# Kernel optimization log

Measured on AMD Instinct MI355X. Metric: run time of the kernel, lower is better.

Reference implementation:

```python
import jax, jax.numpy as jnp
import numpy as np

# loss hyperparameters (module defaults)
ATTENTION_COEFF = 1.0
GAMMA = 0.5
BETA = 8.0
DICE_COEFF = 2500.0
REV_DICE_COEFF = 2500.0
IOU_COEFF = 0.0
EPS = 1e-14
SMOOTH = 1e-6
LOG_CLAMP = -100.0  # torch F.binary_cross_entropy clamps log terms at -100


def setup_inputs() -> dict:
    key = jax.random.key(0)
    k1, k2 = jax.random.split(key)
    B, C, H, W = 16, 4, 512, 512
    cls_score = jax.random.uniform(k1, (B, C, H, W), dtype=jnp.float32)
    label = jax.random.randint(k2, (B, C, H, W), 0, 2, dtype=jnp.int32)
    return {"cls_score": cls_score, "label": label}


def _attention_bce(pred, t):
    # per-batch alpha = num_neg / total over all 4 channels (vectorized over batch)
    num_pos = jnp.sum(t, axis=(1, 2, 3))                      # (B,)
    total = jnp.float32(t.shape[1] * t.shape[2] * t.shape[3])
    alpha = ((total - num_pos) / total)[:, None, None, None]  # (B,1,1,1)
    p_clip = jnp.clip(pred, EPS, 1.0 - EPS)
    # beta ** ((1-p)**gamma) and beta ** (p**gamma)
    w = (t * alpha * BETA ** ((1.0 - p_clip) ** GAMMA)
         + (1.0 - t) * (1.0 - alpha) * BETA ** (p_clip ** GAMMA))
    w = jax.lax.stop_gradient(w)
    # BCE on raw pred, with torch-style log clamping
    log_p = jnp.maximum(jnp.log(pred), LOG_CLAMP)
    log_1mp = jnp.maximum(jnp.log(1.0 - pred), LOG_CLAMP)
    bce = -(t * log_p + (1.0 - t) * log_1mp)
    return jnp.sum(w * bce)


def _dice(pred, t):
    inter = jnp.sum(pred * t, axis=(2, 3))                    # (B,4)
    denom = jnp.sum(pred * pred, axis=(2, 3)) + jnp.sum(t * t, axis=(2, 3))
    return jnp.sum(1.0 - (2.0 * inter + SMOOTH) / (denom + SMOOTH))


def _iou(pred, t):
    inter = jnp.sum(pred * t, axis=(2, 3))
    union = jnp.sum(pred + t, axis=(2, 3)) - inter
    return jnp.sum(1.0 - (inter + SMOOTH) / (union + SMOOTH))


def reference(cls_score, label):
    t = label.astype(jnp.float32)  # (B,4,H,W)
    loss = ATTENTION_COEFF * _attention_bce(cls_score, t)
    loss = loss + DICE_COEFF * _dice(cls_score, t)
    loss = loss + REV_DICE_COEFF * _dice(1.0 - cls_score, 1.0 - t)
    loss = loss + IOU_COEFF * _iou(cls_score, t)
    return loss
```

## Files before the change

### kernel.cpp

```cpp
#include <hip/hip_runtime.h>


typedef float f32x4 __attribute__((ext_vector_type(4)));
typedef int   i32x4 __attribute__((ext_vector_type(4)));

#define B_DIM 16
#define C_DIM 4
#define HW 262144
#define NPLANES 64
#define NTHREADS 128
#define NWAVES (NTHREADS / 64)
#define CHUNK 2048
#define K_CHUNKS (HW / CHUNK)
#define NBLOCKS (NPLANES * K_CHUNKS)
#define NSUMS 6
#define WELEMS (CHUNK / NWAVES)
#define WOPS (WELEMS / 256)

__global__ __launch_bounds__(NTHREADS) void loss_main(
    const float* __restrict__ pred, const int* __restrict__ label,
    float* __restrict__ ws) {
  __shared__ float sp[NWAVES][WELEMS];
  __shared__ int   st[NWAVES][WELEMS];
  __shared__ float red[NWAVES][NSUMS];

  const int block = blockIdx.x;
  const int tid = threadIdx.x;
  const int w = tid >> 6, l = tid & 63;
  const long wbase = (long)block * CHUNK + (long)w * WELEMS;
  const float* gp = pred + wbase;
  const int*   gt = label + wbase;

#pragma unroll
  for (int r = 0; r < WOPS; ++r) {
    __builtin_amdgcn_global_load_lds(
        (const __attribute__((address_space(1))) void*)(gp + r * 256 + l * 4),
        (__attribute__((address_space(3))) void*)(&sp[w][r * 256]), 16, 0, 0);
    __builtin_amdgcn_global_load_lds(
        (const __attribute__((address_space(1))) void*)(gt + r * 256 + l * 4),
        (__attribute__((address_space(3))) void*)(&st[w][r * 256]), 16, 0, 0);
  }
  __syncthreads();

  float s_pt = 0.f, s_pp = 0.f, s_p = 0.f;
  float nsum_t = 0.f;
  float nsum_1 = 0.f;
  int   s_ti = 0;

#pragma unroll
  for (int r = 0; r < WOPS; ++r) {
    f32x4 P = *(const f32x4*)&sp[w][r * 256 + l * 4];
    i32x4 T = *(const i32x4*)&st[w][r * 256 + l * 4];
#pragma unroll
    for (int j = 0; j < 4; ++j) {
      float pv = P[j];
      float tf = (float)T[j];
      float u   = __builtin_fmaf(tf, -2.0f, 1.0f);
      float arg = __builtin_fmaf(pv, u, tf);
      float x   = 1.0f - arg;
      float r_  = __builtin_amdgcn_sqrtf(x);
      float Bw  = __builtin_amdgcn_exp2f(3.0f * r_);
      float lg  = __builtin_amdgcn_logf(arg);
      float L   = fmaxf(0.69314718056f * lg, -100.0f);
      float c   = Bw * (-L);
      nsum_t += c;
      nsum_1  = __builtin_fmaf(tf, c, nsum_1);
      s_pt    = __builtin_fmaf(tf, pv, s_pt);
      s_pp    = __builtin_fmaf(pv, pv, s_pp);
      s_p    += pv;
      s_ti   += T[j];
    }
  }

  float s_t = (float)s_ti;

  float vals[NSUMS] = {s_pt, s_pp, s_t, s_p, nsum_1, nsum_t};
#pragma unroll
  for (int q = 0; q < NSUMS; ++q) {
    float v = vals[q];
#pragma unroll
    for (int off = 32; off; off >>= 1) v += __shfl_down(v, off);
    vals[q] = v;
  }
  if (l == 0) {
#pragma unroll
    for (int q = 0; q < NSUMS; ++q) red[w][q] = vals[q];
  }
  __syncthreads();
  if (tid < NSUMS) {
    float v = 0.f;
#pragma unroll
    for (int ww = 0; ww < NWAVES; ++ww) v += red[ww][tid];
    ws[block * NSUMS + tid] = v;
  }
}

__global__ __launch_bounds__(1024) void loss_finalize(
    const float* __restrict__ ws, float* __restrict__ out) {
  __shared__ float ps[NPLANES][NSUMS];
  const int tid = threadIdx.x;
  const int p = tid >> 4;
  const int s = tid & 15;

  float acc[NSUMS] = {0.f, 0.f, 0.f, 0.f, 0.f, 0.f};
  const f32x4* base =
      (const f32x4*)(ws + (long)p * (K_CHUNKS * NSUMS) + s * 48);
#pragma unroll
  for (int i = 0; i < 12; ++i) {
    f32x4 v = base[i];
#pragma unroll
    for (int j = 0; j < 4; ++j) acc[(i * 4 + j) % 6] += v[j];
  }
#pragma unroll
  for (int q = 0; q < NSUMS; ++q) {
    float v = acc[q];
    v += __shfl_xor(v, 1);
    v += __shfl_xor(v, 2);
    v += __shfl_xor(v, 4);
    v += __shfl_xor(v, 8);
    acc[q] = v;
  }
  if (s == 0) {
#pragma unroll
    for (int q = 0; q < NSUMS; ++q) ps[p][q] = acc[q];
  }
  __syncthreads();

  if (tid < 64) {
    const int pl = tid;
    const float s_pt = ps[pl][0], s_pp = ps[pl][1], s_t = ps[pl][2],
                s_p = ps[pl][3];
    const float sum1 = ps[pl][4];
    const float sum2 = ps[pl][5] - ps[pl][4];
    const float N = (float)HW;
    const float SM = 1e-6f;

    float dice = 1.0f - (2.0f * s_pt + SM) / (s_pp + s_t + SM);
    float inter2 = N - s_p - s_t + s_pt;
    float denom2 = 2.0f * N - 2.0f * s_p + s_pp - s_t;
    float rdice = 1.0f - (2.0f * inter2 + SM) / (denom2 + SM);

    float np4 = s_t + __shfl_xor(s_t, 1);
    np4 += __shfl_xor(np4, 2);
    const float total = (float)(C_DIM * HW);
    float alpha = (total - np4) / total;

    float val = alpha * sum1 + (1.0f - alpha) * sum2
              + 2500.0f * (dice + rdice);

#pragma unroll
    for (int off = 32; off; off >>= 1) val += __shfl_down(val, off);
    if (pl == 0) out[0] = val;
  }
}

extern "C" void kernel_launch(void* const* d_in, const int* in_sizes, int n_in,
                              void* d_out, int out_size, void* d_ws, size_t ws_size,
                              hipStream_t stream) {
  const float* pred = (const float*)d_in[0];
  const int* label = (const int*)d_in[1];
  float* out = (float*)d_out;
  float* ws = (float*)d_ws;

  loss_main<<<NBLOCKS, NTHREADS, 0, stream>>>(pred, label, ws);
  loss_finalize<<<1, 1024, 0, stream>>>(ws, out);
}
```

Before: 31.18 us.

## Double-buffer LDS tiles so each block streams four chunks

Each block now processes four 2048-element tiles instead of one. Asynchronous global-to-LDS loads feed two LDS buffers, so the next tile's loads are in flight while the current tile is computed. This cuts the block count by four and shrinks the per-plane partial-sum array the finalize kernel reduces. In exchange, per-block LDS doubles to about 32KB, which limits how many blocks fit on a CU. The barrier at the end of each iteration may also serialize the loads and the compute.

```diff
diff --git a/kernel.cpp b/kernel.cpp
--- a/kernel.cpp
+++ b/kernel.cpp
@@ -10,67 +10,88 @@
 #define NPLANES 64
 #define NTHREADS 128
 #define NWAVES (NTHREADS / 64)
-#define CHUNK 2048
-#define K_CHUNKS (HW / CHUNK)
-#define NBLOCKS (NPLANES * K_CHUNKS)
+#define TILE 2048
+#define TILES 4
+#define NBLOCKS 2048
+#define BPP 32
 #define NSUMS 6
-#define WELEMS (CHUNK / NWAVES)
+#define WELEMS (TILE / NWAVES)
 #define WOPS (WELEMS / 256)
 
 __global__ __launch_bounds__(NTHREADS) void loss_main(
     const float* __restrict__ pred, const int* __restrict__ label,
     float* __restrict__ ws) {
-  __shared__ float sp[NWAVES][WELEMS];
-  __shared__ int   st[NWAVES][WELEMS];
+  __shared__ float sp[2][TILE];
+  __shared__ int   st[2][TILE];
   __shared__ float red[NWAVES][NSUMS];
 
   const int block = blockIdx.x;
   const int tid = threadIdx.x;
   const int w = tid >> 6, l = tid & 63;
-  const long wbase = (long)block * CHUNK + (long)w * WELEMS;
-  const float* gp = pred + wbase;
-  const int*   gt = label + wbase;
+  const long base0 = (long)block * (TILE * TILES);
+  const float* gp = pred + base0 + w * WELEMS;
+  const int*   gt = label + base0 + w * WELEMS;
 
-#pragma unroll
-  for (int r = 0; r < WOPS; ++r) {
-    __builtin_amdgcn_global_load_lds(
-        (const __attribute__((address_space(1))) void*)(gp + r * 256 + l * 4),
-        (__attribute__((address_space(3))) void*)(&sp[w][r * 256]), 16, 0, 0);
-    __builtin_amdgcn_global_load_lds(
-        (const __attribute__((address_space(1))) void*)(gt + r * 256 + l * 4),
-        (__attribute__((address_space(3))) void*)(&st[w][r * 256]), 16, 0, 0);
+#define STAGE(c, t)                                                          \
+  _Pragma("unroll")                                                          \
+  for (int r = 0; r < WOPS; ++r) {                                           \
+    __builtin_amdgcn_global_load_lds(                                        \
+        (const __attribute__((address_space(1))) void*)(gp + (t) * TILE +    \
+                                                        r * 256 + l * 4),    \
+        (__attribute__((address_space(3))) void*)(&sp[c][w * WELEMS +        \
+                                                         r * 256]),          \
+        16, 0, 0);                                                           \
+    __builtin_amdgcn_global_load_lds(                                        \
+        (const __attribute__((address_space(1))) void*)(gt + (t) * TILE +    \
+                                                        r * 256 + l * 4),    \
+        (__attribute__((address_space(3))) void*)(&st[c][w * WELEMS +        \
+                                                         r * 256]),          \
+        16, 0, 0);                                                           \
   }
-  __syncthreads();
 
   float s_pt = 0.f, s_pp = 0.f, s_p = 0.f;
   float nsum_t = 0.f;
   float nsum_1 = 0.f;
   int   s_ti = 0;
 
+#define COMPUTE(c)                                                           \
+  _Pragma("unroll")                                                          \
+  for (int r = 0; r < WOPS; ++r) {                                           \
+    f32x4 P = *(const f32x4*)&sp[c][w * WELEMS + r * 256 + l * 4];           \
+    i32x4 T = *(const i32x4*)&st[c][w * WELEMS + r * 256 + l * 4];           \
+    _Pragma("unroll")                                                        \
+    for (int j = 0; j < 4; ++j) {                                            \
+      float pv = P[j];                                                       \
+      float tf = (float)T[j];                                \
+      float u   = __builtin_fmaf(tf, -2.0f, 1.0f);                 \
+      float arg = __builtin_fmaf(pv, u, tf);                \
+      float x   = 1.0f - arg;                               \
+      float r_  = __builtin_amdgcn_sqrtf(x);                                 \
+      float Bw  = __builtin_amdgcn_exp2f(3.0f * r_);          \
+      float lg  = __builtin_amdgcn_logf(arg);                      \
+      float L   = fmaxf(0.69314718056f * lg, -100.0f);                       \
+      float cc  = Bw * (-L);                                                 \
+      nsum_t += cc;                                                          \
+      nsum_1  = __builtin_fmaf(tf, cc, nsum_1);                              \
+      s_pt    = __builtin_fmaf(tf, pv, s_pt);                                \
+      s_pp    = __builtin_fmaf(pv, pv, s_pp);                                \
+      s_p    += pv;                                                          \
+      s_ti   += T[j];                                                        \
+    }                                                                        \
+  }
+
+  STAGE(0, 0)
+  __syncthreads();
 #pragma unroll
-  for (int r = 0; r < WOPS; ++r) {
-    f32x4 P = *(const f32x4*)&sp[w][r * 256 + l * 4];
-    i32x4 T = *(const i32x4*)&st[w][r * 256 + l * 4];
-#pragma unroll
-    for (int j = 0; j < 4; ++j) {
-      float pv = P[j];
-      float tf = (float)T[j];
-      float u   = __builtin_fmaf(tf, -2.0f, 1.0f);
-      float arg = __builtin_fmaf(pv, u, tf);
-      float x   = 1.0f - arg;
-      float r_  = __builtin_amdgcn_sqrtf(x);
-      float Bw  = __builtin_amdgcn_exp2f(3.0f * r_);
-      float lg  = __builtin_amdgcn_logf(arg);
-      float L   = fmaxf(0.69314718056f * lg, -100.0f);
-      float c   = Bw * (-L);
-      nsum_t += c;
-      nsum_1  = __builtin_fmaf(tf, c, nsum_1);
-      s_pt    = __builtin_fmaf(tf, pv, s_pt);
-      s_pp    = __builtin_fmaf(pv, pv, s_pp);
-      s_p    += pv;
-      s_ti   += T[j];
-    }
+  for (int t = 0; t < TILES; ++t) {
+    const int cur = t & 1;
+    if (t + 1 < TILES) { STAGE(cur ^ 1, t + 1) }
+    COMPUTE(cur)
+    __syncthreads();
   }
+
+#undef STAGE
+#undef COMPUTE
 
   float s_t = (float)s_ti;
 
@@ -103,10 +124,9 @@
   const int s = tid & 15;
 
   float acc[NSUMS] = {0.f, 0.f, 0.f, 0.f, 0.f, 0.f};
-  const f32x4* base =
-      (const f32x4*)(ws + (long)p * (K_CHUNKS * NSUMS) + s * 48);
+  const f32x4* base = (const f32x4*)(ws + (long)p * (BPP * NSUMS) + s * 12);
 #pragma unroll
-  for (int i = 0; i < 12; ++i) {
+  for (int i = 0; i < 3; ++i) {
     f32x4 v = base[i];
 #pragma unroll
     for (int j = 0; j < 4; ++j) acc[(i * 4 + j) % 6] += v[j];
```

Result: slower. 32.62 us (+4.6%).
